# Kernel tuning notes

Measured on AMD Instinct MI355X. Metric: run time of the kernel, lower is better.

Reference implementation:

```python
import jax, jax.numpy as jnp
import numpy as np

B, T, OB, AC, OBL, ACL, W = 2048, 128, 64, 8, 32, 16, 64
DT = 0.05   # spacing of save times
K = 2       # fixed Dopri5 substeps per interval (step size = ode_dt0 = 0.025)


def _mlp2(x, W0, b0, W1, b1):
    # eqx.nn.MLP with depth=1: in -> width (relu) -> out (identity)
    return jax.nn.relu(x @ W0.T + b0) @ W1.T + b1


def setup_inputs() -> dict:
    key = jax.random.key(0)
    ks = jax.random.split(key, 10)
    def lin(k, o, i, scale=1.0):
        return (jax.random.normal(k, (o, i), jnp.float32) * (scale / np.sqrt(i))).astype(jnp.float32)
    return {
        "encW0": lin(ks[0], W, OB), "encb0": jnp.zeros((W,), jnp.float32),
        "encW1": lin(ks[1], OBL, W), "encb1": jnp.zeros((OBL,), jnp.float32),
        "acW0": lin(ks[2], W, AC), "acb0": jnp.zeros((W,), jnp.float32),
        "acW1": lin(ks[3], ACL, W), "acb1": jnp.zeros((ACL,), jnp.float32),
        "dynW0": lin(ks[4], W, OBL + ACL), "dynb0": jnp.zeros((W,), jnp.float32),
        "dynW1": lin(ks[5], OBL, W, 0.5), "dynb1": jnp.zeros((OBL,), jnp.float32),
        "decW0": lin(ks[6], W, OBL), "decb0": jnp.zeros((W,), jnp.float32),
        "decW1": lin(ks[7], OB, W), "decb1": jnp.zeros((OB,), jnp.float32),
        "ob": jax.random.normal(ks[8], (B, OB), jnp.float32),
        "acs": jax.random.normal(ks[9], (B, T, AC), jnp.float32),
        "times": jnp.tile(jnp.arange(T, dtype=jnp.float32) * DT, (B, 1)),
    }


def _dopri5_step(f, t, y, h):
    k1 = f(t, y)
    k2 = f(t + h * (1. / 5.), y + h * ((1. / 5.) * k1))
    k3 = f(t + h * (3. / 10.), y + h * ((3. / 40.) * k1 + (9. / 40.) * k2))
    k4 = f(t + h * (4. / 5.), y + h * ((44. / 45.) * k1 - (56. / 15.) * k2 + (32. / 9.) * k3))
    k5 = f(t + h * (8. / 9.), y + h * ((19372. / 6561.) * k1 - (25360. / 2187.) * k2
                                       + (64448. / 6561.) * k3 - (212. / 729.) * k4))
    k6 = f(t + h, y + h * ((9017. / 3168.) * k1 - (355. / 33.) * k2 + (46732. / 5247.) * k3
                           + (49. / 176.) * k4 - (5103. / 18656.) * k5))
    return y + h * ((35. / 384.) * k1 + (500. / 1113.) * k3 + (125. / 192.) * k4
                    - (2187. / 6784.) * k5 + (11. / 84.) * k6)


def reference(encW0, encb0, encW1, encb1, acW0, acb0, acW1, acb1,
              dynW0, dynb0, dynW1, dynb1, decW0, decb0, decW1, decb1,
              ob, acs, times):
    ac_latents = _mlp2(acs, acW0, acb0, acW1, acb1)   # (B, T, ACL)
    y0 = _mlp2(ob, encW0, encb0, encW1, encb1)        # (B, OBL)

    def single(y0_i, acl_i, t_i):
        n = t_i.shape[0]

        def f(t, y):
            # piecewise-constant action latent: index of save-interval containing t
            idx = jnp.clip(jnp.searchsorted(t_i, t, side='right') - 1, 0, n - 1)
            return _mlp2(jnp.concatenate([y, acl_i[idx]]), dynW0, dynb0, dynW1, dynb1)

        def interval(y, tt):
            t0, t1 = tt
            h = (t1 - t0) / K
            def sub(yc, j):
                return _dopri5_step(f, t0 + j * h, yc, h), None
            y, _ = jax.lax.scan(sub, y, jnp.arange(K, dtype=t_i.dtype))
            return y, y

        _, ys = jax.lax.scan(interval, y0_i, (t_i[:-1], t_i[1:]))
        return jnp.concatenate([y0_i[None], ys], axis=0)   # (T, OBL)

    ys = jax.vmap(single)(y0, ac_latents, times)            # (B, T, OBL)
    return _mlp2(ys, decW0, decb0, decW1, decb1)            # (B, T, OB)
```

## Files before the change

### kernel.cpp

```cpp
#include <hip/hip_runtime.h>

#define NB 2048
#define NT 128

typedef float v2f __attribute__((ext_vector_type(2)));

static __device__ __forceinline__ v2f pkfma(v2f a, v2f b, v2f c) {
#if __has_builtin(__builtin_elementwise_fma)
    return __builtin_elementwise_fma(a, b, c);
#else
    v2f r; r.x = fmaf(a.x, b.x, c.x); r.y = fmaf(a.y, b.y, c.y); return r;
#endif
}
static __device__ __forceinline__ v2f mkv2(float x, float y) { v2f r; r.x = x; r.y = y; return r; }

template<int CTRL>
static __device__ __forceinline__ float dppf(float v) {
    return __int_as_float(__builtin_amdgcn_update_dpp(
        __float_as_int(v), __float_as_int(v), CTRL, 0xF, 0xF, false));
}
#define DPP_QP1 0xB1
#define DPP_QP2 0x4E
#define DPP_HM  0x141
#define DPP_MIR 0x140

__global__ __launch_bounds__(256, 4) void acl_kernel(
    const float* __restrict__ acs, const float* __restrict__ acW0,
    const float* __restrict__ acb0, const float* __restrict__ acW1,
    const float* __restrict__ acb1, float* __restrict__ aclout)
{
    __shared__ float sW0[64 * 8];
    __shared__ float sW1[16 * 64];
    __shared__ float sB0[64];
    __shared__ float sB1[16];
    const int tid = threadIdx.x;
    for (int i = tid; i < 64 * 8; i += 256) sW0[i] = acW0[i];
    for (int i = tid; i < 16 * 64; i += 256) sW1[i] = acW1[i];
    if (tid < 64) sB0[tid] = acb0[tid];
    if (tid < 16) sB1[tid] = acb1[tid];
    __syncthreads();

    const int row = blockIdx.x * 256 + tid;
    const float4 x0 = *(const float4*)&acs[row * 8];
    const float4 x1 = *(const float4*)&acs[row * 8 + 4];

    float o[16];
    #pragma unroll
    for (int m = 0; m < 16; ++m) o[m] = sB1[m];

    #pragma unroll
    for (int jc = 0; jc < 16; ++jc) {
        float hq[4];
        #pragma unroll
        for (int u = 0; u < 4; ++u) {
            const int j = jc * 4 + u;
            const float4 wa = *(const float4*)&sW0[j * 8];
            const float4 wb = *(const float4*)&sW0[j * 8 + 4];
            float hv = sB0[j];
            hv = fmaf(x0.x, wa.x, hv); hv = fmaf(x0.y, wa.y, hv);
            hv = fmaf(x0.z, wa.z, hv); hv = fmaf(x0.w, wa.w, hv);
            hv = fmaf(x1.x, wb.x, hv); hv = fmaf(x1.y, wb.y, hv);
            hv = fmaf(x1.z, wb.z, hv); hv = fmaf(x1.w, wb.w, hv);
            hq[u] = fmaxf(hv, 0.f);
        }
        #pragma unroll
        for (int m = 0; m < 16; ++m) {
            const float4 wv = *(const float4*)&sW1[m * 64 + jc * 4];
            o[m] = fmaf(hq[0], wv.x, o[m]);
            o[m] = fmaf(hq[1], wv.y, o[m]);
            o[m] = fmaf(hq[2], wv.z, o[m]);
            o[m] = fmaf(hq[3], wv.w, o[m]);
        }
    }
    float4* op = (float4*)&aclout[row * 16];
    op[0] = make_float4(o[0],  o[1],  o[2],  o[3]);
    op[1] = make_float4(o[4],  o[5],  o[6],  o[7]);
    op[2] = make_float4(o[8],  o[9],  o[10], o[11]);
    op[3] = make_float4(o[12], o[13], o[14], o[15]);
}

__global__ __launch_bounds__(256, 2) void ode_kernel(
    const float* __restrict__ encW0, const float* __restrict__ encb0,
    const float* __restrict__ encW1, const float* __restrict__ encb1,
    const float* __restrict__ dynW0, const float* __restrict__ dynb0,
    const float* __restrict__ dynW1, const float* __restrict__ dynb1,
    const float* __restrict__ ob,    const float* __restrict__ times,
    const float* __restrict__ aclws, float* __restrict__ yio)
{
    __shared__ float sEncW0T[64 * 64];
    __shared__ float sEncW1T[64 * 32];
    __shared__ float sW0s[64 * 32];
    __shared__ float sW1T[64 * 32];
    __shared__ float sM[64 * 64];
    __shared__ float sEncB0[64], sEncB1[32], sB1d[32];
    __shared__ float xbuf[4][64];
    __shared__ float hbuf[4][64];
    __shared__ float tbuf[4][NT];

    const int tid = threadIdx.x;
    for (int i = tid; i < 64 * 64; i += 256) { int r = i >> 6, c = i & 63; sEncW0T[c * 64 + r] = encW0[i]; }
    for (int i = tid; i < 32 * 64; i += 256) { int r = i >> 6, c = i & 63; sEncW1T[c * 32 + r] = encW1[i]; }
    for (int i = tid; i < 64 * 32; i += 256) { int j = i >> 5, mm = i & 31; sW0s[i] = dynW0[j * 48 + mm]; }
    for (int i = tid; i < 64 * 32; i += 256) { int c = i >> 5, mm = i & 31; sW1T[i] = dynW1[mm * 64 + c]; }
    if (tid < 64) { sEncB0[tid] = encb0[tid]; }
    if (tid < 32) { sEncB1[tid] = encb1[tid]; sB1d[tid] = dynb1[tid]; }
    __syncthreads();

    {
        const int j  = tid >> 2;
        const int cg = (tid & 3) * 16;
        float4 wr[8];
        #pragma unroll
        for (int q = 0; q < 8; ++q) wr[q] = *(const float4*)&sW0s[j * 32 + q * 4];
        #pragma unroll 2
        for (int k = 0; k < 16; ++k) {
            const int c = cg + k;
            v2f s0 = mkv2(0.f, 0.f), s1 = mkv2(0.f, 0.f);
            #pragma unroll
            for (int q = 0; q < 8; ++q) {
                const float4 t4 = *(const float4*)&sW1T[c * 32 + q * 4];
                s0 = pkfma(mkv2(t4.x, t4.y), mkv2(wr[q].x, wr[q].y), s0);
                s1 = pkfma(mkv2(t4.z, t4.w), mkv2(wr[q].z, wr[q].w), s1);
            }
            sM[j * 64 + c] = (s0.x + s1.x) + (s0.y + s1.y);
        }
    }
    __syncthreads();

    const int w    = tid >> 6;
    const int lane = tid & 63;
    const int bu   = __builtin_amdgcn_readfirstlane(blockIdx.x * 4 + w);
    const int m    = lane & 31;
    const int H    = lane & 32;
    const int rb   = lane & 48;
    const int off  = lane & 15;

    float* __restrict__ xb = xbuf[w];
    float* __restrict__ hb = hbuf[w];

    constexpr int XT[8][2] = {{0,1},{2,3},{7,6},{5,4},{15,14},{13,12},{8,9},{10,11}};

    v2f WM0[8], WM1[8], WM2[8], WM3[8];
    #pragma unroll
    for (int q = 0; q < 8; ++q) {
        const int c0 = rb | (off ^ XT[q][0]);
        const int c1 = rb | (off ^ XT[q][1]);
        WM0[q] = mkv2(sM[lane * 64 + c0],        sM[lane * 64 + c1]);
        WM1[q] = mkv2(sM[(lane ^ 16) * 64 + c0], sM[(lane ^ 16) * 64 + c1]);
        WM2[q] = mkv2(sM[(lane ^ 32) * 64 + c0], sM[(lane ^ 32) * 64 + c1]);
        WM3[q] = mkv2(sM[(lane ^ 48) * 64 + c0], sM[(lane ^ 48) * 64 + c1]);
    }
    v2f V10[8], V11[8];
    #pragma unroll
    for (int q = 0; q < 8; ++q) {
        const int c0 = rb | (off ^ XT[q][0]);
        const int c1 = rb | (off ^ XT[q][1]);
        V10[q] = mkv2(dynW1[m * 64 + c0],        dynW1[m * 64 + c1]);
        V11[q] = mkv2(dynW1[(m ^ 16) * 64 + c0], dynW1[(m ^ 16) * 64 + c1]);
    }
    float wa[16];
    #pragma unroll
    for (int q = 0; q < 4; ++q) *(float4*)&wa[q * 4] = *(const float4*)&dynW0[lane * 48 + 32 + q * 4];
    const float b0r = dynb0[lane];
    const float b1r = dynb1[m];

    tbuf[w][lane]      = times[bu * NT + lane];
    tbuf[w][64 + lane] = times[bu * NT + 64 + lane];
    __builtin_amdgcn_wave_barrier();

    auto gather = [&](float h, v2f* G) {
        G[0] = mkv2(h,                     dppf<DPP_QP1>(h));
        G[1] = mkv2(dppf<DPP_QP2>(G[0].x), dppf<DPP_QP2>(G[0].y));
        G[2] = mkv2(dppf<DPP_HM >(G[0].x), dppf<DPP_HM >(G[0].y));
        G[3] = mkv2(dppf<DPP_HM >(G[1].x), dppf<DPP_HM >(G[1].y));
        G[4] = mkv2(dppf<DPP_MIR>(G[0].x), dppf<DPP_MIR>(G[0].y));
        G[5] = mkv2(dppf<DPP_MIR>(G[1].x), dppf<DPP_MIR>(G[1].y));
        G[6] = mkv2(dppf<DPP_MIR>(G[2].x), dppf<DPP_MIR>(G[2].y));
        G[7] = mkv2(dppf<DPP_MIR>(G[3].x), dppf<DPP_MIR>(G[3].y));
    };

    auto gproj = [&](float h, float vjv) -> float {
        v2f G[8];
        gather(h, G);
        v2f P0 = mkv2(0.f, 0.f), P1 = mkv2(0.f, 0.f);
        v2f P2 = mkv2(0.f, 0.f), P3 = mkv2(0.f, 0.f);
        #pragma unroll
        for (int q = 0; q < 8; ++q) {
            P0 = pkfma(G[q], WM0[q], P0);
            P1 = pkfma(G[q], WM1[q], P1);
            P2 = pkfma(G[q], WM2[q], P2);
            P3 = pkfma(G[q], WM3[q], P3);
        }
        const float p0 = P0.x + P0.y, p1 = P1.x + P1.y;
        const float p2 = P2.x + P2.y, p3 = P3.x + P3.y;
        const float u  = p0 + __shfl_xor(p1, 16, 64);
        const float vv = p2 + __shfl_xor(p3, 16, 64);
        return u + __shfl_xor(vv, 32, 64) + vjv;
    };

    float y;
    {
        xb[lane] = ob[bu * 64 + lane];
        __builtin_amdgcn_wave_barrier();
        float4 xv[16];
        #pragma unroll
        for (int q = 0; q < 16; ++q) xv[q] = *(const float4*)&xb[q * 4];
        float a0 = sEncB0[lane], a1 = 0.f, a2 = 0.f, a3 = 0.f;
        #pragma unroll
        for (int q = 0; q < 16; ++q) {
            a0 = fmaf(xv[q].x, sEncW0T[(q * 4 + 0) * 64 + lane], a0);
            a1 = fmaf(xv[q].y, sEncW0T[(q * 4 + 1) * 64 + lane], a1);
            a2 = fmaf(xv[q].z, sEncW0T[(q * 4 + 2) * 64 + lane], a2);
            a3 = fmaf(xv[q].w, sEncW0T[(q * 4 + 3) * 64 + lane], a3);
        }
        const float hj = fmaxf((a0 + a1) + (a2 + a3), 0.f);
        hb[lane] = hj;
        __builtin_amdgcn_wave_barrier();
        float4 hv[8];
        #pragma unroll
        for (int q = 0; q < 8; ++q) hv[q] = *(const float4*)&hb[H + q * 4];
        float c0 = 0.f, c1 = 0.f, c2 = 0.f, c3 = 0.f;
        #pragma unroll
        for (int q = 0; q < 8; ++q) {
            c0 = fmaf(hv[q].x, sEncW1T[(H + q * 4 + 0) * 32 + m], c0);
            c1 = fmaf(hv[q].y, sEncW1T[(H + q * 4 + 1) * 32 + m], c1);
            c2 = fmaf(hv[q].z, sEncW1T[(H + q * 4 + 2) * 32 + m], c2);
            c3 = fmaf(hv[q].w, sEncW1T[(H + q * 4 + 3) * 32 + m], c3);
        }
        float part = (c0 + c1) + (c2 + c3);
        part += __shfl_xor(part, 32, 64);
        y = part + sEncB1[m];
    }

    float ystar = 0.f, vj = 0.f;
    {
        __builtin_amdgcn_wave_barrier();
        xb[m] = y;
        __builtin_amdgcn_wave_barrier();
        #pragma unroll
        for (int q = 0; q < 8; ++q) {
            const float4 wv = *(const float4*)&dynW0[lane * 48 + q * 4];
            const float4 xv = *(const float4*)&xb[q * 4];
            ystar = fmaf(wv.x, xv.x, ystar); ystar = fmaf(wv.y, xv.y, ystar);
            ystar = fmaf(wv.z, xv.z, ystar); ystar = fmaf(wv.w, xv.w, ystar);
            vj = fmaf(wv.x, sB1d[q * 4 + 0], vj); vj = fmaf(wv.y, sB1d[q * 4 + 1], vj);
            vj = fmaf(wv.z, sB1d[q * 4 + 2], vj); vj = fmaf(wv.w, sB1d[q * 4 + 3], vj);
        }
    }

    auto acl_part = [&](const float* __restrict__ ap) -> float {
        float ar[16];
        #pragma unroll
        for (int q = 0; q < 4; ++q) *(float4*)&ar[q * 4] = *(const float4*)&ap[q * 4];
        const v2f* a2 = (const v2f*)ar;
        const v2f* wq = (const v2f*)wa;
        v2f s0 = mkv2(0.f, 0.f), s1 = mkv2(0.f, 0.f);
        #pragma unroll
        for (int q = 0; q < 8; q += 2) {
            s0 = pkfma(a2[q],     wq[q],     s0);
            s1 = pkfma(a2[q + 1], wq[q + 1], s1);
        }
        const v2f s = s0 + s1;
        return s.x + s.y;
    };

    auto store_y = [&](float yv, int t) {
        if (lane < 32) yio[(size_t)(bu * NT + t) * 64 + lane] = yv;
    };

    float aclPartC = acl_part(aclws + (size_t)(bu * NT) * 16);
    store_y(y, 0);

    for (int i = 0; i < NT - 1; ++i) {
        const float t0v = tbuf[w][i];
        const float t1v = tbuf[w][i + 1];
        const float hh  = (t1v - t0v) * 0.5f;
        const float aclPartN = acl_part(aclws + (size_t)(bu * NT + i + 1) * 16);
        float haccS = 0.f;

        #pragma unroll 1
        for (int sub = 0; sub < 2; ++sub) {
            const float tsub  = t0v + (float)sub * hh;
            const bool  swap6 = (tsub + hh >= t1v);

            const float a1v = ystar + b0r + aclPartC;

            const float h1 = fmaxf(a1v, 0.f);
            const float g1 = hh * gproj(h1, vj);
            const float h2 = fmaxf(fmaf(0.2f, g1, a1v), 0.f);
            const float g2 = hh * gproj(h2, vj);
            const float h3 = fmaxf(fmaf(0.075f, g1, fmaf(0.225f, g2, a1v)), 0.f);
            const float g3 = hh * gproj(h3, vj);
            const float h4 = fmaxf(
                fmaf((float)(44.0/45.0), g1,
                fmaf((float)(-56.0/15.0), g2,
                fmaf((float)(32.0/9.0), g3, a1v))), 0.f);
            const float g4 = hh * gproj(h4, vj);
            const float h5 = fmaxf(
                fmaf((float)(19372.0/6561.0), g1,
                fmaf((float)(-25360.0/2187.0), g2,
                fmaf((float)(64448.0/6561.0), g3,
                fmaf((float)(-212.0/729.0), g4, a1v)))), 0.f);
            const float g5 = hh * gproj(h5, vj);
            float a6v =
                fmaf((float)(9017.0/3168.0), g1,
                fmaf((float)(-355.0/33.0), g2,
                fmaf((float)(46732.0/5247.0), g3,
                fmaf((float)(49.0/176.0), g4,
                fmaf((float)(-5103.0/18656.0), g5, a1v)))));
            a6v += swap6 ? (aclPartN - aclPartC) : 0.f;
            const float h6 = fmaxf(a6v, 0.f);

            float ha = (float)(35.0/384.0) * h1;
            ha = fmaf((float)(500.0/1113.0),   h3, ha);
            ha = fmaf((float)(125.0/192.0),    h4, ha);
            ha = fmaf((float)(-2187.0/6784.0), h5, ha);
            ha = fmaf((float)(11.0/84.0),      h6, ha);

            const float gacc = gproj(ha, vj);
            ystar = fmaf(hh, gacc, ystar);
            haccS += ha;
        }

        {
            v2f G[8];
            gather(haccS, G);
            v2f P0 = mkv2(0.f, 0.f), P1 = mkv2(0.f, 0.f);
            #pragma unroll
            for (int q = 0; q < 8; ++q) {
                P0 = pkfma(G[q], V10[q], P0);
                P1 = pkfma(G[q], V11[q], P1);
            }
            const float p0 = P0.x + P0.y, p1 = P1.x + P1.y;
            const float u  = p0 + __shfl_xor(p1, 16, 64);
            const float gf = u + __shfl_xor(u, 32, 64);
            y = fmaf(hh, gf + 2.f * b1r, y);
        }
        aclPartC = aclPartN;
        store_y(y, i + 1);
    }
}

__global__ __launch_bounds__(256, 2) void dec_kernel(
    const float* __restrict__ decW0, const float* __restrict__ decb0,
    const float* __restrict__ decW1, const float* __restrict__ decb1,
    float* __restrict__ yio)
{
    __shared__ float sW0[64 * 32];
    __shared__ float sW1T[64 * 64];
    __shared__ float sB0[64];
    __shared__ float sB1[64];
    const int tid = threadIdx.x;
    for (int i = tid; i < 64 * 32; i += 256) sW0[i] = decW0[i];
    for (int i = tid; i < 64 * 64; i += 256) { int n = i >> 6, j = i & 63; sW1T[j * 64 + n] = decW1[i]; }
    if (tid < 64) { sB0[tid] = decb0[tid]; sB1[tid] = decb1[tid]; }
    __syncthreads();

    const size_t row = (size_t)blockIdx.x * 256 + tid;
    float* rp = &yio[row * 64];

    float xr[32];
    #pragma unroll
    for (int q = 0; q < 8; ++q) *(float4*)&xr[q * 4] = *(const float4*)&rp[q * 4];

    v2f o2[32];
    #pragma unroll
    for (int n = 0; n < 32; ++n) o2[n] = mkv2(sB1[2 * n], sB1[2 * n + 1]);

    #pragma unroll 4
    for (int j = 0; j < 64; ++j) {
        v2f a0 = mkv2(sB0[j], 0.f), a1 = mkv2(0.f, 0.f);
        #pragma unroll
        for (int q = 0; q < 8; ++q) {
            const float4 wv = *(const float4*)&sW0[j * 32 + q * 4];
            a0 = pkfma(*(const v2f*)&xr[q * 4],     mkv2(wv.x, wv.y), a0);
            a1 = pkfma(*(const v2f*)&xr[q * 4 + 2], mkv2(wv.z, wv.w), a1);
        }
        const float hj = fmaxf((a0.x + a1.x) + (a0.y + a1.y), 0.f);
        const v2f h2 = mkv2(hj, hj);
        #pragma unroll
        for (int q = 0; q < 16; ++q) {
            const float4 wv = *(const float4*)&sW1T[j * 64 + q * 4];
            o2[2 * q]     = pkfma(h2, mkv2(wv.x, wv.y), o2[2 * q]);
            o2[2 * q + 1] = pkfma(h2, mkv2(wv.z, wv.w), o2[2 * q + 1]);
        }
    }

    #pragma unroll
    for (int q = 0; q < 16; ++q)
        *(float4*)&rp[q * 4] = make_float4(o2[2 * q].x, o2[2 * q].y,
                                           o2[2 * q + 1].x, o2[2 * q + 1].y);
}

extern "C" void kernel_launch(void* const* d_in, const int* in_sizes, int n_in,
                              void* d_out, int out_size, void* d_ws, size_t ws_size,
                              hipStream_t stream)
{
    const float* encW0 = (const float*)d_in[0];
    const float* encb0 = (const float*)d_in[1];
    const float* encW1 = (const float*)d_in[2];
    const float* encb1 = (const float*)d_in[3];
    const float* acW0  = (const float*)d_in[4];
    const float* acb0  = (const float*)d_in[5];
    const float* acW1  = (const float*)d_in[6];
    const float* acb1  = (const float*)d_in[7];
    const float* dynW0 = (const float*)d_in[8];
    const float* dynb0 = (const float*)d_in[9];
    const float* dynW1 = (const float*)d_in[10];
    const float* dynb1 = (const float*)d_in[11];
    const float* decW0 = (const float*)d_in[12];
    const float* decb0 = (const float*)d_in[13];
    const float* decW1 = (const float*)d_in[14];
    const float* decb1 = (const float*)d_in[15];
    const float* ob    = (const float*)d_in[16];
    const float* acs   = (const float*)d_in[17];
    const float* times = (const float*)d_in[18];
    float* out = (float*)d_out;
    float* acl = (float*)d_ws;

    acl_kernel<<<(NB * NT) / 256, 256, 0, stream>>>(acs, acW0, acb0, acW1, acb1, acl);
    ode_kernel<<<NB / 4, 256, 0, stream>>>(encW0, encb0, encW1, encb1,
                                           dynW0, dynb0, dynW1, dynb1,
                                           ob, times, acl, out);
    dec_kernel<<<(NB * NT) / 256, 256, 0, stream>>>(decW0, decb0, decW1, decb1, out);
}
```

Measured before the change: 726.9 us.

## Replace DPP gather with LDS broadcast and recompute pre-activation from y each substep

Drops the DPP-based cross-lane gather in the projection helper and broadcasts hidden activations through per-wave LDS instead, loading contiguous float4 slices. It also stops propagating the hidden-space state (ystar) and projecting the summed ha once per interval. Each substep now rebuilds the pre-activation directly from y with a dynW0 matvec and updates y after every substep. This removes one gproj per substep and the DPP chains, at the cost of an extra matvec, LDS round-trips and wave barriers on the serial critical path.

```diff
diff --git a/kernel.cpp b/kernel.cpp
--- a/kernel.cpp
+++ b/kernel.cpp
@@ -13,16 +13,6 @@
 #endif
 }
 static __device__ __forceinline__ v2f mkv2(float x, float y) { v2f r; r.x = x; r.y = y; return r; }
-
-template<int CTRL>
-static __device__ __forceinline__ float dppf(float v) {
-    return __int_as_float(__builtin_amdgcn_update_dpp(
-        __float_as_int(v), __float_as_int(v), CTRL, 0xF, 0xF, false));
-}
-#define DPP_QP1 0xB1
-#define DPP_QP2 0x4E
-#define DPP_HM  0x141
-#define DPP_MIR 0x140
 
 __global__ __launch_bounds__(256, 4) void acl_kernel(
     const float* __restrict__ acs, const float* __restrict__ acW0,
@@ -133,63 +123,75 @@
     const int m    = lane & 31;
     const int H    = lane & 32;
     const int rb   = lane & 48;
-    const int off  = lane & 15;
+    const int yq   = (lane & 48) >> 1;
 
     float* __restrict__ xb = xbuf[w];
     float* __restrict__ hb = hbuf[w];
 
-    constexpr int XT[8][2] = {{0,1},{2,3},{7,6},{5,4},{15,14},{13,12},{8,9},{10,11}};
-
-    v2f WM0[8], WM1[8], WM2[8], WM3[8];
-    #pragma unroll
-    for (int q = 0; q < 8; ++q) {
-        const int c0 = rb | (off ^ XT[q][0]);
-        const int c1 = rb | (off ^ XT[q][1]);
-        WM0[q] = mkv2(sM[lane * 64 + c0],        sM[lane * 64 + c1]);
-        WM1[q] = mkv2(sM[(lane ^ 16) * 64 + c0], sM[(lane ^ 16) * 64 + c1]);
-        WM2[q] = mkv2(sM[(lane ^ 32) * 64 + c0], sM[(lane ^ 32) * 64 + c1]);
-        WM3[q] = mkv2(sM[(lane ^ 48) * 64 + c0], sM[(lane ^ 48) * 64 + c1]);
-    }
-    v2f V10[8], V11[8];
-    #pragma unroll
-    for (int q = 0; q < 8; ++q) {
-        const int c0 = rb | (off ^ XT[q][0]);
-        const int c1 = rb | (off ^ XT[q][1]);
-        V10[q] = mkv2(dynW1[m * 64 + c0],        dynW1[m * 64 + c1]);
-        V11[q] = mkv2(dynW1[(m ^ 16) * 64 + c0], dynW1[(m ^ 16) * 64 + c1]);
-    }
+    float WM0f[16], WM1f[16], WM2f[16], WM3f[16];
+    #pragma unroll
+    for (int q = 0; q < 4; ++q) {
+        *(float4*)&WM0f[q * 4] = *(const float4*)&sM[lane * 64 + rb + q * 4];
+        *(float4*)&WM1f[q * 4] = *(const float4*)&sM[(lane ^ 16) * 64 + rb + q * 4];
+        *(float4*)&WM2f[q * 4] = *(const float4*)&sM[(lane ^ 32) * 64 + rb + q * 4];
+        *(float4*)&WM3f[q * 4] = *(const float4*)&sM[(lane ^ 48) * 64 + rb + q * 4];
+    }
+    const v2f* WM0 = (const v2f*)WM0f; const v2f* WM1 = (const v2f*)WM1f;
+    const v2f* WM2 = (const v2f*)WM2f; const v2f* WM3 = (const v2f*)WM3f;
+
+    float W0Af[8], W0Bf[8], W0Cf[8], W0Df[8];
+    #pragma unroll
+    for (int q = 0; q < 2; ++q) {
+        *(float4*)&W0Af[q * 4] = *(const float4*)&dynW0[lane * 48 + yq + q * 4];
+        *(float4*)&W0Bf[q * 4] = *(const float4*)&dynW0[(lane ^ 16) * 48 + yq + q * 4];
+        *(float4*)&W0Cf[q * 4] = *(const float4*)&dynW0[(lane ^ 32) * 48 + yq + q * 4];
+        *(float4*)&W0Df[q * 4] = *(const float4*)&dynW0[(lane ^ 48) * 48 + yq + q * 4];
+    }
+    const v2f* W0A = (const v2f*)W0Af; const v2f* W0B = (const v2f*)W0Bf;
+    const v2f* W0C = (const v2f*)W0Cf; const v2f* W0D = (const v2f*)W0Df;
+
+    float V10f[16], V11f[16];
+    #pragma unroll
+    for (int q = 0; q < 4; ++q) {
+        *(float4*)&V10f[q * 4] = *(const float4*)&dynW1[m * 64 + rb + q * 4];
+        *(float4*)&V11f[q * 4] = *(const float4*)&dynW1[(m ^ 16) * 64 + rb + q * 4];
+    }
+    const v2f* V10 = (const v2f*)V10f; const v2f* V11 = (const v2f*)V11f;
+
     float wa[16];
     #pragma unroll
     for (int q = 0; q < 4; ++q) *(float4*)&wa[q * 4] = *(const float4*)&dynW0[lane * 48 + 32 + q * 4];
     const float b0r = dynb0[lane];
     const float b1r = dynb1[m];
 
+    float vj = 0.f;
+    #pragma unroll
+    for (int q = 0; q < 8; ++q) {
+        const float4 wv = *(const float4*)&dynW0[lane * 48 + q * 4];
+        vj = fmaf(wv.x, sB1d[q * 4 + 0], vj); vj = fmaf(wv.y, sB1d[q * 4 + 1], vj);
+        vj = fmaf(wv.z, sB1d[q * 4 + 2], vj); vj = fmaf(wv.w, sB1d[q * 4 + 3], vj);
+    }
+
     tbuf[w][lane]      = times[bu * NT + lane];
     tbuf[w][64 + lane] = times[bu * NT + 64 + lane];
     __builtin_amdgcn_wave_barrier();
 
-    auto gather = [&](float h, v2f* G) {
-        G[0] = mkv2(h,                     dppf<DPP_QP1>(h));
-        G[1] = mkv2(dppf<DPP_QP2>(G[0].x), dppf<DPP_QP2>(G[0].y));
-        G[2] = mkv2(dppf<DPP_HM >(G[0].x), dppf<DPP_HM >(G[0].y));
-        G[3] = mkv2(dppf<DPP_HM >(G[1].x), dppf<DPP_HM >(G[1].y));
-        G[4] = mkv2(dppf<DPP_MIR>(G[0].x), dppf<DPP_MIR>(G[0].y));
-        G[5] = mkv2(dppf<DPP_MIR>(G[1].x), dppf<DPP_MIR>(G[1].y));
-        G[6] = mkv2(dppf<DPP_MIR>(G[2].x), dppf<DPP_MIR>(G[2].y));
-        G[7] = mkv2(dppf<DPP_MIR>(G[3].x), dppf<DPP_MIR>(G[3].y));
-    };
-
-    auto gproj = [&](float h, float vjv) -> float {
-        v2f G[8];
-        gather(h, G);
+    auto gproj = [&](float hsv, float vjv) -> float {
+        __builtin_amdgcn_wave_barrier();
+        hb[lane] = hsv;
+        __builtin_amdgcn_wave_barrier();
+        float hr[16];
+        #pragma unroll
+        for (int q = 0; q < 4; ++q) *(float4*)&hr[q * 4] = *(const float4*)&hb[rb + q * 4];
+        const v2f* hp = (const v2f*)hr;
         v2f P0 = mkv2(0.f, 0.f), P1 = mkv2(0.f, 0.f);
         v2f P2 = mkv2(0.f, 0.f), P3 = mkv2(0.f, 0.f);
         #pragma unroll
         for (int q = 0; q < 8; ++q) {
-            P0 = pkfma(G[q], WM0[q], P0);
-            P1 = pkfma(G[q], WM1[q], P1);
-            P2 = pkfma(G[q], WM2[q], P2);
-            P3 = pkfma(G[q], WM3[q], P3);
+            P0 = pkfma(hp[q], WM0[q], P0);
+            P1 = pkfma(hp[q], WM1[q], P1);
+            P2 = pkfma(hp[q], WM2[q], P2);
+            P3 = pkfma(hp[q], WM3[q], P3);
         }
         const float p0 = P0.x + P0.y, p1 = P1.x + P1.y;
         const float p2 = P2.x + P2.y, p3 = P3.x + P3.y;
@@ -232,22 +234,6 @@
         y = part + sEncB1[m];
     }
 
-    float ystar = 0.f, vj = 0.f;
-    {
-        __builtin_amdgcn_wave_barrier();
-        xb[m] = y;
-        __builtin_amdgcn_wave_barrier();
-        #pragma unroll
-        for (int q = 0; q < 8; ++q) {
-            const float4 wv = *(const float4*)&dynW0[lane * 48 + q * 4];
-            const float4 xv = *(const float4*)&xb[q * 4];
-            ystar = fmaf(wv.x, xv.x, ystar); ystar = fmaf(wv.y, xv.y, ystar);
-            ystar = fmaf(wv.z, xv.z, ystar); ystar = fmaf(wv.w, xv.w, ystar);
-            vj = fmaf(wv.x, sB1d[q * 4 + 0], vj); vj = fmaf(wv.y, sB1d[q * 4 + 1], vj);
-            vj = fmaf(wv.z, sB1d[q * 4 + 2], vj); vj = fmaf(wv.w, sB1d[q * 4 + 3], vj);
-        }
-    }
-
     auto acl_part = [&](const float* __restrict__ ap) -> float {
         float ar[16];
         #pragma unroll
@@ -276,14 +262,36 @@
         const float t1v = tbuf[w][i + 1];
         const float hh  = (t1v - t0v) * 0.5f;
         const float aclPartN = acl_part(aclws + (size_t)(bu * NT + i + 1) * 16);
-        float haccS = 0.f;
 
         #pragma unroll 1
         for (int sub = 0; sub < 2; ++sub) {
             const float tsub  = t0v + (float)sub * hh;
             const bool  swap6 = (tsub + hh >= t1v);
 
-            const float a1v = ystar + b0r + aclPartC;
+            __builtin_amdgcn_wave_barrier();
+            xb[m] = y;
+            __builtin_amdgcn_wave_barrier();
+            float a1v;
+            {
+                float xr[8];
+                *(float4*)&xr[0] = *(const float4*)&xb[yq];
+                *(float4*)&xr[4] = *(const float4*)&xb[yq + 4];
+                const v2f* xp = (const v2f*)xr;
+                v2f A0 = mkv2(0.f, 0.f), A1 = mkv2(0.f, 0.f);
+                v2f A2 = mkv2(0.f, 0.f), A3 = mkv2(0.f, 0.f);
+                #pragma unroll
+                for (int q = 0; q < 4; ++q) {
+                    A0 = pkfma(xp[q], W0A[q], A0);
+                    A1 = pkfma(xp[q], W0B[q], A1);
+                    A2 = pkfma(xp[q], W0C[q], A2);
+                    A3 = pkfma(xp[q], W0D[q], A3);
+                }
+                const float q0 = A0.x + A0.y, q1 = A1.x + A1.y;
+                const float q2 = A2.x + A2.y, q3 = A3.x + A3.y;
+                const float u  = q0 + __shfl_xor(q1, 16, 64);
+                const float vv = q2 + __shfl_xor(q3, 16, 64);
+                a1v = u + __shfl_xor(vv, 32, 64) + b0r + aclPartC;
+            }
 
             const float h1 = fmaxf(a1v, 0.f);
             const float g1 = hh * gproj(h1, vj);
@@ -317,24 +325,25 @@
             ha = fmaf((float)(-2187.0/6784.0), h5, ha);
             ha = fmaf((float)(11.0/84.0),      h6, ha);
 
-            const float gacc = gproj(ha, vj);
-            ystar = fmaf(hh, gacc, ystar);
-            haccS += ha;
-        }
-
-        {
-            v2f G[8];
-            gather(haccS, G);
-            v2f P0 = mkv2(0.f, 0.f), P1 = mkv2(0.f, 0.f);
-            #pragma unroll
-            for (int q = 0; q < 8; ++q) {
-                P0 = pkfma(G[q], V10[q], P0);
-                P1 = pkfma(G[q], V11[q], P1);
+            __builtin_amdgcn_wave_barrier();
+            hb[lane] = ha;
+            __builtin_amdgcn_wave_barrier();
+            {
+                float hr[16];
+                #pragma unroll
+                for (int q = 0; q < 4; ++q) *(float4*)&hr[q * 4] = *(const float4*)&hb[rb + q * 4];
+                const v2f* hp = (const v2f*)hr;
+                v2f P0 = mkv2(0.f, 0.f), P1 = mkv2(0.f, 0.f);
+                #pragma unroll
+                for (int q = 0; q < 8; ++q) {
+                    P0 = pkfma(hp[q], V10[q], P0);
+                    P1 = pkfma(hp[q], V11[q], P1);
+                }
+                const float p0 = P0.x + P0.y, p1 = P1.x + P1.y;
+                const float u  = p0 + __shfl_xor(p1, 16, 64);
+                const float full = u + __shfl_xor(u, 32, 64);
+                y = fmaf(hh, full + b1r, y);
             }
-            const float p0 = P0.x + P0.y, p1 = P1.x + P1.y;
-            const float u  = p0 + __shfl_xor(p1, 16, 64);
-            const float gf = u + __shfl_xor(u, 32, 64);
-            y = fmaf(hh, gf + 2.f * b1r, y);
         }
         aclPartC = aclPartN;
         store_y(y, i + 1);
```

Result: faster. 622.8 us (-14.3%).
